# Kernel tuning notes

Measured on AMD Instinct MI355X. Metric: run time of the kernel, lower is better.

The kernel has to match this reference:

```python
import jax, jax.numpy as jnp
import numpy as np

N_Q = 4       # n_qubits
PATCH = 3
PAD = 1       # patch_size // 2


def _u3(theta, phi, lam):
    # U3 gate matrix (2x2 complex)
    c = jnp.cos(theta / 2)
    s = jnp.sin(theta / 2)
    row0 = jnp.stack([c + 0j, -jnp.exp(1j * lam) * s])
    row1 = jnp.stack([jnp.exp(1j * phi) * s, jnp.exp(1j * (phi + lam)) * c])
    return jnp.stack([row0, row1]).astype(jnp.complex64)


def _apply_1q(state, U, wire):
    # state: (N,2,2,2,2) complex; U: (2,2) shared or (N,2,2) batched
    s = jnp.moveaxis(state, 1 + wire, -1)
    shp = s.shape
    s = s.reshape(s.shape[0], -1, 2)
    if U.ndim == 2:
        out = jnp.einsum('ij,nrj->nri', U, s)
    else:
        out = jnp.einsum('nij,nrj->nri', U, s)
    return jnp.moveaxis(out.reshape(shp), -1, 1 + wire)


def _apply_2q(state, U4, cw, tw):
    # U4: (4,4) on (control, target) subspace ordered |c t>
    s = jnp.moveaxis(state, (1 + cw, 1 + tw), (-2, -1))
    shp = s.shape
    s = s.reshape(s.shape[0], -1, 4)
    out = jnp.einsum('ij,nrj->nri', U4, s)
    return jnp.moveaxis(out.reshape(shp), (-2, -1), (1 + cw, 1 + tw))


def setup_inputs() -> dict:
    key = jax.random.key(0)
    ks = jax.random.split(key, 8)
    B, C, H, W = 16, 64, 64, 64
    out_ch = 128
    d_in = C * PATCH * PATCH  # 576
    x = jax.random.normal(ks[0], (B, C, H, W), dtype=jnp.float32)
    fc1_w = jax.random.normal(ks[1], (N_Q, d_in), dtype=jnp.float32) * (1.0 / np.sqrt(d_in))
    fc1_b = jax.random.normal(ks[2], (N_Q,), dtype=jnp.float32) * 0.01
    u3_params = jax.random.normal(ks[3], (N_Q, 3), dtype=jnp.float32)
    cu3_params = jax.random.normal(ks[4], (N_Q, 3), dtype=jnp.float32)
    fc_w = jax.random.normal(ks[5], (out_ch, N_Q), dtype=jnp.float32) * 0.5
    fc_b = jax.random.normal(ks[6], (out_ch,), dtype=jnp.float32) * 0.01
    return {"x": x, "fc1_w": fc1_w, "fc1_b": fc1_b, "u3_params": u3_params,
            "cu3_params": cu3_params, "fc_w": fc_w, "fc_b": fc_b}


def reference(x, fc1_w, fc1_b, u3_params, cu3_params, fc_w, fc_b):
    B, C, H, W = x.shape
    xp = jnp.pad(x, ((0, 0), (0, 0), (PAD, PAD), (PAD, PAD)))
    Hout, Wout = H, W  # stride 1, same padding
    # im2col: feature order (C, di, dj) matches torch patch.reshape(B,-1)
    cols = jnp.stack([xp[:, :, di:di + Hout, dj:dj + Wout]
                      for di in range(PATCH) for dj in range(PATCH)], axis=2)  # (B,C,9,H,W)
    patches = cols.transpose(0, 3, 4, 1, 2).reshape(B, Hout * Wout, C * PATCH * PATCH)
    ang = patches @ fc1_w.T + fc1_b  # (B, P, 4) rotation angles
    Np = B * Hout * Wout
    ang = ang.reshape(Np, N_Q)
    # initial state |0000> for every (batch, patch)
    state = jnp.zeros((Np, 2 ** N_Q), jnp.complex64).at[:, 0].set(1.0)
    state = state.reshape((Np,) + (2,) * N_Q)
    # RY encoding (per-element angles)
    for w in range(N_Q):
        th = ang[:, w] / 2
        c, s = jnp.cos(th), jnp.sin(th)
        Ury = jnp.stack([jnp.stack([c, -s], -1), jnp.stack([s, c], -1)], -2).astype(jnp.complex64)
        state = _apply_1q(state, Ury, w)
    # trainable U3 on every wire
    for w in range(N_Q):
        state = _apply_1q(state, _u3(u3_params[w, 0], u3_params[w, 1], u3_params[w, 2]), w)
    # circular CU3 ring (0,1),(1,2),(2,3),(3,0)
    for w in range(N_Q):
        U = _u3(cu3_params[w, 0], cu3_params[w, 1], cu3_params[w, 2])
        U4 = jnp.eye(4, dtype=jnp.complex64).at[2:, 2:].set(U)
        state = _apply_2q(state, U4, w, (w + 1) % N_Q)
    # <Z> on each wire
    probs = state.real ** 2 + state.imag ** 2  # (Np,2,2,2,2)
    zv = jnp.array([1.0, -1.0], jnp.float32)
    expz = jnp.stack(
        [(probs * zv.reshape((1,) + (1,) * w + (2,) + (1,) * (N_Q - 1 - w))).sum(axis=(1, 2, 3, 4))
         for w in range(N_Q)], axis=1)  # (Np,4)
    out = expz.reshape(B, Hout * Wout, N_Q) @ fc_w.T + fc_b  # (B,P,out_ch)
    out_ch = fc_w.shape[0]
    # faithful to original: view(B, out_ch, side_h, side_w) on contiguous (P,out_ch)
    return out.reshape(B, out_ch, Hout, Wout)
```

## Files before the change

### kernel.cpp

```cpp
#include <hip/hip_runtime.h>
#include <hip/hip_bf16.h>
#include <math.h>

typedef unsigned short u16;
typedef unsigned int   u32;
typedef unsigned long long u64;

#define WS_W2    0
#define WS_B4    2304
#define WS_FCW   2308
#define WS_FCB   2820
#define WS_GATES 2948
#define WS_FLAG  3012

__device__ inline float bfbits2f(u32 lo16) {
    u32 u = lo16 << 16;
    return __builtin_bit_cast(float, u);
}
__device__ inline float bchi(u32 w) {
    return __builtin_bit_cast(float, w & 0xffff0000u);
}
__device__ inline float bclo(u32 w) {
    return __builtin_bit_cast(float, w << 16);
}
__device__ inline u16 f2bf(float f) {
    u32 u = __builtin_bit_cast(u32, f);
    u = u + 0x7fffu + ((u >> 16) & 1u);
    return (u16)(u >> 16);
}
__device__ inline float ld_param(const void* p, int i, int isbf16) {
    return isbf16 ? bfbits2f(((const u16*)p)[i]) : ((const float*)p)[i];
}

__global__ __launch_bounds__(256) void k0_prep(
        const void* __restrict__ x,
        const void* __restrict__ fc1_w, const void* __restrict__ fc1_b,
        const void* __restrict__ u3p,   const void* __restrict__ cu3p,
        const void* __restrict__ fc_w,  const void* __restrict__ fc_b,
        float* __restrict__ ws) {
    __shared__ int sflag;
    int t = threadIdx.x;
    if (t == 0) {
        const u32* xw = (const u32*)x;
        int cnt = 0;
        for (int i = 0; i < 64; ++i) {
            u32 e = (xw[i] >> 7) & 0xFFu;
            if (e >= 110 && e <= 130) ++cnt;
        }
        sflag = (cnt >= 32) ? 1 : 0;
        ws[WS_FLAG] = (float)sflag;
    }
    __syncthreads();
    const int bf = sflag;
    for (int idx = t; idx < 2304; idx += 256) {
        int c = idx / 36;
        int rem = idx - c * 36;
        int q = rem / 9;
        int k = rem - q * 9;
        ws[WS_W2 + idx] = ld_param(fc1_w, q * 576 + c * 9 + k, bf);
    }
    if (t < 4)   ws[WS_B4 + t] = ld_param(fc1_b, t, bf);
    for (int idx = t; idx < 512; idx += 256) ws[WS_FCW + idx] = ld_param(fc_w, idx, bf);
    if (t < 128) ws[WS_FCB + t] = ld_param(fc_b, t, bf);
    if (t < 8) {
        int w = t & 3;
        const void* p = (t < 4) ? u3p : cu3p;
        float th = ld_param(p, w * 3 + 0, bf);
        float ph = ld_param(p, w * 3 + 1, bf);
        float la = ld_param(p, w * 3 + 2, bf);
        float c = cosf(0.5f * th), s = sinf(0.5f * th);
        float cl = cosf(la), sl = sinf(la);
        float cp = cosf(ph), sp = sinf(ph);
        float cpl = cp * cl - sp * sl, spl = sp * cl + cp * sl;
        float* m = ws + WS_GATES + t * 8;
        m[0] = c;        m[1] = 0.f;
        m[2] = -cl * s;  m[3] = -sl * s;
        m[4] = cp * s;   m[5] = sp * s;
        m[6] = cpl * c;  m[7] = spl * c;
    }
}

__global__ __launch_bounds__(256) void k1_fused(
        const void* __restrict__ x, const float* __restrict__ ws,
        void* __restrict__ out) {
    __shared__ u32 tile[3 * 64 * 34];
    const int t = threadIdx.x;
    const int b = blockIdx.x >> 6;
    const int row = blockIdx.x & 63;
    const int bf = (ws[WS_FLAG] != 0.0f) ? 1 : 0;

    const u32*    xu = (const u32*)x;
    const float2* xf = (const float2*)x;
    const int xbase = b * 131072;

    {
        const int jj = t & 31;
        const int seed = t >> 5;
#pragma unroll
        for (int i = 0; i < 24; ++i) {
            int rowAll = seed + i * 8;
            int r = rowAll >> 6, c = rowAll & 63;
            int gr = row - 1 + r;
            u32 pk = 0;
            if (gr >= 0 && gr < 64) {
                int idx = xbase + c * 2048 + gr * 32 + jj;
                if (bf) pk = xu[idx];
                else { float2 v = xf[idx];
                       pk = (u32)f2bf(v.x) | ((u32)f2bf(v.y) << 16); }
            }
            tile[rowAll * 34 + 1 + jj] = pk;
        }
        if (t < 192) { tile[t * 34] = 0u; tile[t * 34 + 33] = 0u; }
    }
    __syncthreads();

    const int j = t & 63, cq = t >> 6;
    const int pj = (j + 1) >> 1;
    const int sh = (1 - (j & 1)) * 16;
    float ang0 = 0.f, ang1 = 0.f, ang2 = 0.f, ang3 = 0.f;
#pragma unroll
    for (int cc = 0; cc < 16; ++cc) {
        const int c = cq * 16 + cc;
        const int cs = __builtin_amdgcn_readfirstlane(c);
        const float* wp = ws + WS_W2 + cs * 36;
#pragma unroll
        for (int r = 0; r < 3; ++r) {
            const u32* rp = tile + (r * 64 + c) * 34 + pj;
            u32 lo = rp[0], hi = rp[1];
            u64 v = (((u64)hi << 32) | lo) >> sh;
            u32 vlo = (u32)v, vhi = (u32)(v >> 32);
            float e0 = bclo(vlo);
            float e1 = bchi(vlo);
            float e2 = bclo(vhi);
            const float* w0 = wp + r * 3;
            ang0 += e0 * w0[0]  + e1 * w0[1]  + e2 * w0[2];
            ang1 += e0 * w0[9]  + e1 * w0[10] + e2 * w0[11];
            ang2 += e0 * w0[18] + e1 * w0[19] + e2 * w0[20];
            ang3 += e0 * w0[27] + e1 * w0[28] + e2 * w0[29];
        }
    }

    float* red = (float*)tile;
    __syncthreads();
    *(float4*)&red[(cq * 64 + j) * 4] = make_float4(ang0, ang1, ang2, ang3);
    __syncthreads();

    if (t < 64) {
        const float4 a0 = *(const float4*)&red[t * 4];
        const float4 a1 = *(const float4*)&red[256 + t * 4];
        const float4 a2 = *(const float4*)&red[512 + t * 4];
        const float4 a3 = *(const float4*)&red[768 + t * 4];
        float angf[4];
        angf[0] = ws[WS_B4 + 0] + a0.x + a1.x + a2.x + a3.x;
        angf[1] = ws[WS_B4 + 1] + a0.y + a1.y + a2.y + a3.y;
        angf[2] = ws[WS_B4 + 2] + a0.z + a1.z + a2.z + a3.z;
        angf[3] = ws[WS_B4 + 3] + a0.w + a1.w + a2.w + a3.w;

        const float* G = ws + WS_GATES;
        float vr[4][2], vi[4][2];
#pragma unroll
        for (int w = 0; w < 4; ++w) {
            float sa, ca;
            __sincosf(0.5f * angf[w], &sa, &ca);
            const float* m = G + w * 8;
            vr[w][0] = m[0] * ca + m[2] * sa;  vi[w][0] = m[1] * ca + m[3] * sa;
            vr[w][1] = m[4] * ca + m[6] * sa;  vi[w][1] = m[5] * ca + m[7] * sa;
        }
        float t01r[4], t01i[4], t23r[4], t23i[4];
#pragma unroll
        for (int a = 0; a < 2; ++a)
#pragma unroll
            for (int bq = 0; bq < 2; ++bq) {
                t01r[a * 2 + bq] = vr[0][a] * vr[1][bq] - vi[0][a] * vi[1][bq];
                t01i[a * 2 + bq] = vr[0][a] * vi[1][bq] + vi[0][a] * vr[1][bq];
                t23r[a * 2 + bq] = vr[2][a] * vr[3][bq] - vi[2][a] * vi[3][bq];
                t23i[a * 2 + bq] = vr[2][a] * vi[3][bq] + vi[2][a] * vr[3][bq];
            }
        float ar[16], ai[16];
#pragma unroll
        for (int n = 0; n < 16; ++n) {
            int hi = n >> 2, lo = n & 3;
            ar[n] = t01r[hi] * t23r[lo] - t01i[hi] * t23i[lo];
            ai[n] = t01r[hi] * t23i[lo] + t01i[hi] * t23r[lo];
        }
#pragma unroll
        for (int w = 0; w < 4; ++w) {
            const float* m = G + 32 + w * 8;
            const int cb = 8 >> w;
            const int tb = 8 >> ((w + 1) & 3);
#pragma unroll
            for (int n = 0; n < 16; ++n) {
                if ((n & cb) != 0 && (n & tb) == 0) {
                    int n1 = n | tb;
                    float a0r = ar[n], a0i = ai[n], a1r = ar[n1], a1i = ai[n1];
                    ar[n]  = m[0] * a0r - m[1] * a0i + m[2] * a1r - m[3] * a1i;
                    ai[n]  = m[0] * a0i + m[1] * a0r + m[2] * a1i + m[3] * a1r;
                    ar[n1] = m[4] * a0r - m[5] * a0i + m[6] * a1r - m[7] * a1i;
                    ai[n1] = m[4] * a0i + m[5] * a0r + m[6] * a1i + m[7] * a1r;
                }
            }
        }
        float ez[4] = {0.f, 0.f, 0.f, 0.f};
#pragma unroll
        for (int n = 0; n < 16; ++n) {
            float pr = ar[n] * ar[n] + ai[n] * ai[n];
#pragma unroll
            for (int w = 0; w < 4; ++w)
                ez[w] += ((n >> (3 - w)) & 1) ? -pr : pr;
        }
        *(float4*)&red[1024 + t * 4] = make_float4(ez[0], ez[1], ez[2], ez[3]);
    }
    __syncthreads();

    {
        const int p = t >> 2;
        const int og = (t & 3) * 32;
        const float4 ez = *(const float4*)&red[1024 + p * 4];
        const float4* fw4 = (const float4*)(ws + WS_FCW) + og;
        const float4* fb4 = (const float4*)(ws + WS_FCB + og);
        const long base = (long)(b * 4096 + row * 64 + p) * 128 + og;
        if (bf) {
            uint4* o = (uint4*)((u16*)out + base);
#pragma unroll
            for (int ch = 0; ch < 4; ++ch) {
                float4 w0 = fw4[ch * 8 + 0], w1 = fw4[ch * 8 + 1];
                float4 w2 = fw4[ch * 8 + 2], w3 = fw4[ch * 8 + 3];
                float4 w4 = fw4[ch * 8 + 4], w5 = fw4[ch * 8 + 5];
                float4 w6 = fw4[ch * 8 + 6], w7 = fw4[ch * 8 + 7];
                float4 bA = fb4[ch * 2], bB = fb4[ch * 2 + 1];
                float v0 = bA.x + ez.x*w0.x + ez.y*w0.y + ez.z*w0.z + ez.w*w0.w;
                float v1 = bA.y + ez.x*w1.x + ez.y*w1.y + ez.z*w1.z + ez.w*w1.w;
                float v2 = bA.z + ez.x*w2.x + ez.y*w2.y + ez.z*w2.z + ez.w*w2.w;
                float v3 = bA.w + ez.x*w3.x + ez.y*w3.y + ez.z*w3.z + ez.w*w3.w;
                float v4 = bB.x + ez.x*w4.x + ez.y*w4.y + ez.z*w4.z + ez.w*w4.w;
                float v5 = bB.y + ez.x*w5.x + ez.y*w5.y + ez.z*w5.z + ez.w*w5.w;
                float v6 = bB.z + ez.x*w6.x + ez.y*w6.y + ez.z*w6.z + ez.w*w6.w;
                float v7 = bB.w + ez.x*w7.x + ez.y*w7.y + ez.z*w7.z + ez.w*w7.w;
                u32 p0 = (u32)f2bf(v0) | ((u32)f2bf(v1) << 16);
                u32 p1 = (u32)f2bf(v2) | ((u32)f2bf(v3) << 16);
                u32 p2 = (u32)f2bf(v4) | ((u32)f2bf(v5) << 16);
                u32 p3 = (u32)f2bf(v6) | ((u32)f2bf(v7) << 16);
                o[ch] = make_uint4(p0, p1, p2, p3);
            }
        } else {
            float4* o = (float4*)((float*)out + base);
#pragma unroll
            for (int ch = 0; ch < 4; ++ch) {
                float4 bA = fb4[ch * 2], bB = fb4[ch * 2 + 1];
                float4 r0, r1;
                float4 w0 = fw4[ch * 8 + 0], w1 = fw4[ch * 8 + 1];
                float4 w2 = fw4[ch * 8 + 2], w3 = fw4[ch * 8 + 3];
                float4 w4 = fw4[ch * 8 + 4], w5 = fw4[ch * 8 + 5];
                float4 w6 = fw4[ch * 8 + 6], w7 = fw4[ch * 8 + 7];
                r0.x = bA.x + ez.x*w0.x + ez.y*w0.y + ez.z*w0.z + ez.w*w0.w;
                r0.y = bA.y + ez.x*w1.x + ez.y*w1.y + ez.z*w1.z + ez.w*w1.w;
                r0.z = bA.z + ez.x*w2.x + ez.y*w2.y + ez.z*w2.z + ez.w*w2.w;
                r0.w = bA.w + ez.x*w3.x + ez.y*w3.y + ez.z*w3.z + ez.w*w3.w;
                r1.x = bB.x + ez.x*w4.x + ez.y*w4.y + ez.z*w4.z + ez.w*w4.w;
                r1.y = bB.y + ez.x*w5.x + ez.y*w5.y + ez.z*w5.z + ez.w*w5.w;
                r1.z = bB.z + ez.x*w6.x + ez.y*w6.y + ez.z*w6.z + ez.w*w6.w;
                r1.w = bB.w + ez.x*w7.x + ez.y*w7.y + ez.z*w7.z + ez.w*w7.w;
                o[ch * 2 + 0] = r0;
                o[ch * 2 + 1] = r1;
            }
        }
    }
}

extern "C" void kernel_launch(void* const* d_in, const int* in_sizes, int n_in,
                              void* d_out, int out_size, void* d_ws, size_t ws_size,
                              hipStream_t stream) {
    float* ws = (float*)d_ws;
    k0_prep<<<dim3(1), dim3(256), 0, stream>>>(d_in[0], d_in[1], d_in[2], d_in[3],
                                               d_in[4], d_in[5], d_in[6], ws);
    k1_fused<<<dim3(1024), dim3(256), 0, stream>>>(d_in[0], ws, d_out);
}
```

Measured before the change: 129.2 us.

## Split fused kernel into channel-split conv partials plus separate circuit/FC kernel

Splits the single fused kernel into two. The first splits input channels four ways across 4096 blocks and writes partial angle sums to a workspace buffer. The second reduces those partials, runs the quantum circuit and the output FC layer with a restructured store pattern. The aim is more parallelism and smaller shared-memory use per block in the input-bound conv stage, at the cost of an extra launch and a global round trip for the partials.

```diff
diff --git a/kernel.cpp b/kernel.cpp
--- a/kernel.cpp
+++ b/kernel.cpp
@@ -12,6 +12,7 @@
 #define WS_FCB   2820
 #define WS_GATES 2948
 #define WS_FLAG  3012
+#define WS_PART  4096
 
 __device__ inline float bfbits2f(u32 lo16) {
     u32 u = lo16 << 16;
@@ -80,14 +81,18 @@
     }
 }
 
-__global__ __launch_bounds__(256) void k1_fused(
+__global__ __launch_bounds__(256) void kA_conv(
         const void* __restrict__ x, const float* __restrict__ ws,
-        void* __restrict__ out) {
-    __shared__ u32 tile[3 * 64 * 34];
+        float4* __restrict__ part) {
+    __shared__ u32 tile[3 * 16 * 34];
+    __shared__ float4 red4[256];
     const int t = threadIdx.x;
-    const int b = blockIdx.x >> 6;
-    const int row = blockIdx.x & 63;
+    const int bid = blockIdx.x;
+    const int cg  = bid & 3;
+    const int row = (bid >> 2) & 63;
+    const int b   = bid >> 8;
     const int bf = (ws[WS_FLAG] != 0.0f) ? 1 : 0;
+    const int c0 = cg * 16;
 
     const u32*    xu = (const u32*)x;
     const float2* xf = (const float2*)x;
@@ -95,37 +100,37 @@
 
     {
         const int jj = t & 31;
-        const int seed = t >> 5;
-#pragma unroll
-        for (int i = 0; i < 24; ++i) {
-            int rowAll = seed + i * 8;
-            int r = rowAll >> 6, c = rowAll & 63;
+        const int half = t >> 5;
+#pragma unroll
+        for (int i = 0; i < 6; ++i) {
+            int rowcl = half + i * 8;
+            int r = rowcl >> 4, cl = rowcl & 15;
             int gr = row - 1 + r;
             u32 pk = 0;
             if (gr >= 0 && gr < 64) {
-                int idx = xbase + c * 2048 + gr * 32 + jj;
+                int idx = xbase + (c0 + cl) * 2048 + gr * 32 + jj;
                 if (bf) pk = xu[idx];
                 else { float2 v = xf[idx];
                        pk = (u32)f2bf(v.x) | ((u32)f2bf(v.y) << 16); }
             }
-            tile[rowAll * 34 + 1 + jj] = pk;
-        }
-        if (t < 192) { tile[t * 34] = 0u; tile[t * 34 + 33] = 0u; }
-    }
-    __syncthreads();
-
-    const int j = t & 63, cq = t >> 6;
+            tile[rowcl * 34 + 1 + jj] = pk;
+        }
+        if (t < 96) { int rc = t >> 1; tile[rc * 34 + ((t & 1) ? 33 : 0)] = 0u; }
+    }
+    __syncthreads();
+
+    const int j = t & 63, tc = t >> 6;
     const int pj = (j + 1) >> 1;
     const int sh = (1 - (j & 1)) * 16;
     float ang0 = 0.f, ang1 = 0.f, ang2 = 0.f, ang3 = 0.f;
 #pragma unroll
-    for (int cc = 0; cc < 16; ++cc) {
-        const int c = cq * 16 + cc;
-        const int cs = __builtin_amdgcn_readfirstlane(c);
+    for (int cc = 0; cc < 4; ++cc) {
+        const int cl = tc * 4 + cc;
+        const int cs = __builtin_amdgcn_readfirstlane(c0 + cl);
         const float* wp = ws + WS_W2 + cs * 36;
 #pragma unroll
         for (int r = 0; r < 3; ++r) {
-            const u32* rp = tile + (r * 64 + c) * 34 + pj;
+            const u32* rp = tile + (r * 16 + cl) * 34 + pj;
             u32 lo = rp[0], hi = rp[1];
             u64 v = (((u64)hi << 32) | lo) >> sh;
             u32 vlo = (u32)v, vhi = (u32)(v >> 32);
@@ -140,16 +145,32 @@
         }
     }
 
-    float* red = (float*)tile;
-    __syncthreads();
-    *(float4*)&red[(cq * 64 + j) * 4] = make_float4(ang0, ang1, ang2, ang3);
-    __syncthreads();
-
+    red4[tc * 64 + j] = make_float4(ang0, ang1, ang2, ang3);
+    __syncthreads();
     if (t < 64) {
-        const float4 a0 = *(const float4*)&red[t * 4];
-        const float4 a1 = *(const float4*)&red[256 + t * 4];
-        const float4 a2 = *(const float4*)&red[512 + t * 4];
-        const float4 a3 = *(const float4*)&red[768 + t * 4];
+        float4 a0 = red4[t], a1 = red4[64 + t], a2 = red4[128 + t], a3 = red4[192 + t];
+        float4 s = make_float4(a0.x + a1.x + a2.x + a3.x,
+                               a0.y + a1.y + a2.y + a3.y,
+                               a0.z + a1.z + a2.z + a3.z,
+                               a0.w + a1.w + a2.w + a3.w);
+        part[cg * 65536 + b * 4096 + row * 64 + t] = s;
+    }
+}
+
+__global__ __launch_bounds__(256) void kB_circuit_fc(
+        const float* __restrict__ ws, const float4* __restrict__ part,
+        void* __restrict__ out) {
+    __shared__ float4 smEz[64];
+    const int t = threadIdx.x;
+    const int bp0 = blockIdx.x * 64;
+    const int bf = (ws[WS_FLAG] != 0.0f) ? 1 : 0;
+
+    if (t < 64) {
+        const int bp = bp0 + t;
+        float4 a0 = part[bp];
+        float4 a1 = part[65536 + bp];
+        float4 a2 = part[131072 + bp];
+        float4 a3 = part[196608 + bp];
         float angf[4];
         angf[0] = ws[WS_B4 + 0] + a0.x + a1.x + a2.x + a3.x;
         angf[1] = ws[WS_B4 + 1] + a0.y + a1.y + a2.y + a3.y;
@@ -208,61 +229,39 @@
             for (int w = 0; w < 4; ++w)
                 ez[w] += ((n >> (3 - w)) & 1) ? -pr : pr;
         }
-        *(float4*)&red[1024 + t * 4] = make_float4(ez[0], ez[1], ez[2], ez[3]);
-    }
-    __syncthreads();
-
-    {
-        const int p = t >> 2;
-        const int og = (t & 3) * 32;
-        const float4 ez = *(const float4*)&red[1024 + p * 4];
-        const float4* fw4 = (const float4*)(ws + WS_FCW) + og;
-        const float4* fb4 = (const float4*)(ws + WS_FCB + og);
-        const long base = (long)(b * 4096 + row * 64 + p) * 128 + og;
+        smEz[t] = make_float4(ez[0], ez[1], ez[2], ez[3]);
+    }
+    __syncthreads();
+
+    const int og = (t & 15) * 8;
+    const float4* fw4 = (const float4*)(ws + WS_FCW) + og;
+    const float*  fbp = ws + WS_FCB + og;
+    float4 w0 = fw4[0], w1 = fw4[1], w2 = fw4[2], w3 = fw4[3];
+    float4 w4 = fw4[4], w5 = fw4[5], w6 = fw4[6], w7 = fw4[7];
+    float4 bA = *(const float4*)fbp, bB = *(const float4*)(fbp + 4);
+#pragma unroll
+    for (int ch = 0; ch < 4; ++ch) {
+        const int pl = (t >> 4) + ch * 16;
+        const float4 ez = smEz[pl];
+        float v0 = bA.x + ez.x*w0.x + ez.y*w0.y + ez.z*w0.z + ez.w*w0.w;
+        float v1 = bA.y + ez.x*w1.x + ez.y*w1.y + ez.z*w1.z + ez.w*w1.w;
+        float v2 = bA.z + ez.x*w2.x + ez.y*w2.y + ez.z*w2.z + ez.w*w2.w;
+        float v3 = bA.w + ez.x*w3.x + ez.y*w3.y + ez.z*w3.z + ez.w*w3.w;
+        float v4 = bB.x + ez.x*w4.x + ez.y*w4.y + ez.z*w4.z + ez.w*w4.w;
+        float v5 = bB.y + ez.x*w5.x + ez.y*w5.y + ez.z*w5.z + ez.w*w5.w;
+        float v6 = bB.z + ez.x*w6.x + ez.y*w6.y + ez.z*w6.z + ez.w*w6.w;
+        float v7 = bB.w + ez.x*w7.x + ez.y*w7.y + ez.z*w7.z + ez.w*w7.w;
         if (bf) {
-            uint4* o = (uint4*)((u16*)out + base);
-#pragma unroll
-            for (int ch = 0; ch < 4; ++ch) {
-                float4 w0 = fw4[ch * 8 + 0], w1 = fw4[ch * 8 + 1];
-                float4 w2 = fw4[ch * 8 + 2], w3 = fw4[ch * 8 + 3];
-                float4 w4 = fw4[ch * 8 + 4], w5 = fw4[ch * 8 + 5];
-                float4 w6 = fw4[ch * 8 + 6], w7 = fw4[ch * 8 + 7];
-                float4 bA = fb4[ch * 2], bB = fb4[ch * 2 + 1];
-                float v0 = bA.x + ez.x*w0.x + ez.y*w0.y + ez.z*w0.z + ez.w*w0.w;
-                float v1 = bA.y + ez.x*w1.x + ez.y*w1.y + ez.z*w1.z + ez.w*w1.w;
-                float v2 = bA.z + ez.x*w2.x + ez.y*w2.y + ez.z*w2.z + ez.w*w2.w;
-                float v3 = bA.w + ez.x*w3.x + ez.y*w3.y + ez.z*w3.z + ez.w*w3.w;
-                float v4 = bB.x + ez.x*w4.x + ez.y*w4.y + ez.z*w4.z + ez.w*w4.w;
-                float v5 = bB.y + ez.x*w5.x + ez.y*w5.y + ez.z*w5.z + ez.w*w5.w;
-                float v6 = bB.z + ez.x*w6.x + ez.y*w6.y + ez.z*w6.z + ez.w*w6.w;
-                float v7 = bB.w + ez.x*w7.x + ez.y*w7.y + ez.z*w7.z + ez.w*w7.w;
-                u32 p0 = (u32)f2bf(v0) | ((u32)f2bf(v1) << 16);
-                u32 p1 = (u32)f2bf(v2) | ((u32)f2bf(v3) << 16);
-                u32 p2 = (u32)f2bf(v4) | ((u32)f2bf(v5) << 16);
-                u32 p3 = (u32)f2bf(v6) | ((u32)f2bf(v7) << 16);
-                o[ch] = make_uint4(p0, p1, p2, p3);
-            }
+            u32 p0 = (u32)f2bf(v0) | ((u32)f2bf(v1) << 16);
+            u32 p1 = (u32)f2bf(v2) | ((u32)f2bf(v3) << 16);
+            u32 p2 = (u32)f2bf(v4) | ((u32)f2bf(v5) << 16);
+            u32 p3 = (u32)f2bf(v6) | ((u32)f2bf(v7) << 16);
+            ((uint4*)out)[blockIdx.x * 1024 + ch * 256 + t] =
+                make_uint4(p0, p1, p2, p3);
         } else {
-            float4* o = (float4*)((float*)out + base);
-#pragma unroll
-            for (int ch = 0; ch < 4; ++ch) {
-                float4 bA = fb4[ch * 2], bB = fb4[ch * 2 + 1];
-                float4 r0, r1;
-                float4 w0 = fw4[ch * 8 + 0], w1 = fw4[ch * 8 + 1];
-                float4 w2 = fw4[ch * 8 + 2], w3 = fw4[ch * 8 + 3];
-                float4 w4 = fw4[ch * 8 + 4], w5 = fw4[ch * 8 + 5];
-                float4 w6 = fw4[ch * 8 + 6], w7 = fw4[ch * 8 + 7];
-                r0.x = bA.x + ez.x*w0.x + ez.y*w0.y + ez.z*w0.z + ez.w*w0.w;
-                r0.y = bA.y + ez.x*w1.x + ez.y*w1.y + ez.z*w1.z + ez.w*w1.w;
-                r0.z = bA.z + ez.x*w2.x + ez.y*w2.y + ez.z*w2.z + ez.w*w2.w;
-                r0.w = bA.w + ez.x*w3.x + ez.y*w3.y + ez.z*w3.z + ez.w*w3.w;
-                r1.x = bB.x + ez.x*w4.x + ez.y*w4.y + ez.z*w4.z + ez.w*w4.w;
-                r1.y = bB.y + ez.x*w5.x + ez.y*w5.y + ez.z*w5.z + ez.w*w5.w;
-                r1.z = bB.z + ez.x*w6.x + ez.y*w6.y + ez.z*w6.z + ez.w*w6.w;
-                r1.w = bB.w + ez.x*w7.x + ez.y*w7.y + ez.z*w7.z + ez.w*w7.w;
-                o[ch * 2 + 0] = r0;
-                o[ch * 2 + 1] = r1;
-            }
+            float4* o = (float4*)out + (blockIdx.x * 2048 + ch * 512 + 2 * t);
+            o[0] = make_float4(v0, v1, v2, v3);
+            o[1] = make_float4(v4, v5, v6, v7);
         }
     }
 }
@@ -271,7 +270,9 @@
                               void* d_out, int out_size, void* d_ws, size_t ws_size,
                               hipStream_t stream) {
     float* ws = (float*)d_ws;
+    float4* part = (float4*)(ws + WS_PART);
     k0_prep<<<dim3(1), dim3(256), 0, stream>>>(d_in[0], d_in[1], d_in[2], d_in[3],
                                                d_in[4], d_in[5], d_in[6], ws);
-    k1_fused<<<dim3(1024), dim3(256), 0, stream>>>(d_in[0], ws, d_out);
-}
+    kA_conv<<<dim3(4096), dim3(256), 0, stream>>>(d_in[0], ws, part);
+    kB_circuit_fc<<<dim3(1024), dim3(256), 0, stream>>>(ws, part, d_out);
+}
```

Measured after the change: 110.8 us. 1.17x faster.
